# Optimization experiments

Hardware: AMD Instinct MI355X
Metric: run time of the kernel (lower is better)

The kernel has to match this reference:

```python
import jax, jax.numpy as jnp
import numpy as np

B, S, D = 2, 2048, 2048
HQ, HKV, HD = 32, 8, 64
G = HQ // HKV  # groups = 4


def _rope_freqs(seq_len, head_dim):
    # standard RoPE angles: theta_i = 10000^(-2i/d), angle[t,i] = t*theta_i
    inv = 1.0 / (10000.0 ** (np.arange(0, head_dim, 2, dtype=np.float32) / head_dim))
    ang = np.arange(seq_len, dtype=np.float32)[:, None] * inv[None, :]  # [S, HD/2]
    cos = np.cos(ang)[None, :, None, :]  # [1, S, 1, HD/2]
    sin = np.sin(ang)[None, :, None, :]
    return jnp.asarray(cos), jnp.asarray(sin)


def setup_inputs() -> dict:
    key = jax.random.key(0)
    ks = jax.random.split(key, 5)
    freq_cos, freq_sin = _rope_freqs(S, HD)
    scale_in = 1.0 / np.sqrt(D)
    return {
        "x": jax.random.normal(ks[0], (B, S, D), dtype=jnp.float32),
        "freq_cos": freq_cos,
        "freq_sin": freq_sin,
        "wq": jax.random.normal(ks[1], (D, HQ * HD), dtype=jnp.float32) * scale_in,
        "wk": jax.random.normal(ks[2], (D, HKV * HD), dtype=jnp.float32) * scale_in,
        "wv": jax.random.normal(ks[3], (D, HKV * HD), dtype=jnp.float32) * scale_in,
        "wo": jax.random.normal(ks[4], (HQ * HD, D), dtype=jnp.float32) * scale_in,
    }


def _apply_rope(x, cos, sin):
    # x: [b, s, h, hd]; treat last dim as hd/2 complex pairs (interleaved)
    b, s, h, d = x.shape
    xr = x[..., 0::2]  # real parts [b,s,h,hd/2]
    xi = x[..., 1::2]  # imag parts
    or_ = xr * cos - xi * sin
    oi_ = xr * sin + xi * cos
    return jnp.stack([or_, oi_], axis=-1).reshape(b, s, h, d)


def reference(x, freq_cos, freq_sin, wq, wk, wv, wo):
    b, s, d = x.shape
    q = (x @ wq).reshape(b, s, HQ, HD)
    k = (x @ wk).reshape(b, s, HKV, HD)
    v = (x @ wv).reshape(b, s, HKV, HD)
    q = _apply_rope(q, freq_cos[:, :s], freq_sin[:, :s])
    k = _apply_rope(k, freq_cos[:, :s], freq_sin[:, :s])
    # group query heads by kv head: [b, hkv, g, s, hd]
    q = q.transpose(0, 2, 1, 3).reshape(b, HKV, G, s, HD)
    k = k.transpose(0, 2, 1, 3)  # [b, hkv, s, hd]
    v = v.transpose(0, 2, 1, 3)  # [b, hkv, s, hd]
    scores = jnp.einsum("bkgqd,bktd->bkgqt", q, k)
    causal = jnp.tril(jnp.ones((s, s), dtype=bool))
    scores = jnp.where(causal, scores, -jnp.inf)
    attn = jax.nn.softmax(scores / np.sqrt(HD).astype(np.float32), axis=-1)
    out = jnp.einsum("bkgqt,bktd->bkgqd", attn, v)
    out = out.reshape(b, HQ, s, HD).transpose(0, 2, 1, 3).reshape(b, s, d)
    return out @ wo
```

## Files before the change

kernel.cpp:

```cpp
#include <hip/hip_runtime.h>

#define DEVI __device__ __forceinline__

typedef _Float16 h16;
typedef h16 h16x8 __attribute__((ext_vector_type(8)));
typedef h16 h16x4 __attribute__((ext_vector_type(4)));
typedef float f32x4 __attribute__((ext_vector_type(4)));
typedef unsigned short u16;
typedef u16 u16x8 __attribute__((ext_vector_type(8)));
typedef u16 u16x4 __attribute__((ext_vector_type(4)));

constexpr int Bc = 2, Sc = 2048, Dc = 2048, HQc = 32, HKVc = 8, HDc = 64;

DEVI u16 f2h(float f){ h16 h = (h16)f; return __builtin_bit_cast(u16, h); }
DEVI float h2f(u16 u){ return (float)__builtin_bit_cast(h16, u); }

DEVI f32x4 mfma32(h16x8 a, h16x8 b, f32x4 c){ return __builtin_amdgcn_mfma_f32_16x16x32_f16(a, b, c, 0, 0, 0); }
DEVI f32x4 mfma16(h16x4 a, h16x4 b, f32x4 c){ return __builtin_amdgcn_mfma_f32_16x16x16f16(a, b, c, 0, 0, 0); }

DEVI void glds16(const void* g, void* l){
  __builtin_amdgcn_global_load_lds((__attribute__((address_space(1))) void*)g,
                                   (__attribute__((address_space(3))) void*)l, 16, 0, 0);
}

__global__ __launch_bounds__(256) void convert_x(const float* __restrict__ src, u16* __restrict__ dst){
  size_t i = ((size_t)blockIdx.x * 256 + threadIdx.x) * 8;
  f32x4 a = *(const f32x4*)(src + i);
  f32x4 b = *(const f32x4*)(src + i + 4);
  u16x8 o;
  #pragma unroll
  for (int j = 0; j < 4; ++j){ o[j] = f2h(a[j]); o[4+j] = f2h(b[j]); }
  *(u16x8*)(dst + i) = o;
}

__global__ __launch_bounds__(256) void transpose_w(const float* __restrict__ wq, const float* __restrict__ wk,
                                                   const float* __restrict__ wv, const float* __restrict__ wo,
                                                   u16* __restrict__ wqT, u16* __restrict__ wkT,
                                                   u16* __restrict__ wvT, u16* __restrict__ woT){
  __shared__ float tile[32][33];
  int z = blockIdx.z;
  const float* src = (z==0) ? wq : (z==1) ? wk : (z==2) ? wv : wo;
  u16* dst         = (z==0) ? wqT : (z==1) ? wkT : (z==2) ? wvT : woT;
  int N = (z==0 || z==3) ? 2048 : 512;
  int n0 = blockIdx.x * 32;
  if (n0 >= N) return;
  int k0 = blockIdx.y * 32;
  int tx = threadIdx.x, ty = threadIdx.y;
  #pragma unroll
  for (int i = 0; i < 4; ++i)
    tile[ty + i*8][tx] = src[(size_t)(k0 + ty + i*8) * N + n0 + tx];
  __syncthreads();
  #pragma unroll
  for (int i = 0; i < 4; ++i){
    int nn = ty + i*8;
    dst[(size_t)(n0 + nn) * 2048 + k0 + tx] = f2h(tile[tx][nn]);
  }
}

template<int MODE>
__global__ __launch_bounds__(256) void gemm_k(const u16* __restrict__ A,
    const u16* __restrict__ W0, const u16* __restrict__ W1, const u16* __restrict__ W2,
    u16* __restrict__ Qb, u16* __restrict__ Kb, u16* __restrict__ Vb, float* __restrict__ Out){
  __shared__ u16 ldsA[128 * 64];
  __shared__ u16 ldsB[128 * 64];
  int tid = threadIdx.x, wv_ = tid >> 6, l = tid & 63, t = l & 15, g = l >> 4;
  int wm = wv_ >> 1, wn = wv_ & 1;
  int m0 = blockIdx.y * 128, n0 = blockIdx.x * 128;
  const u16* Wt; int n0l; int matid;
  if (MODE == 1){ Wt = W0; n0l = n0; matid = 0; }
  else {
    if (n0 < 2048)      { Wt = W0; n0l = n0;        matid = 0; }
    else if (n0 < 2560) { Wt = W1; n0l = n0 - 2048; matid = 1; }
    else                { Wt = W2; n0l = n0 - 2560; matid = 2; }
  }
  f32x4 acc[4][4] = {};
  int lr = l >> 3, lc = l & 7;
  for (int kk = 0; kk < 32; ++kk){
    int k0 = kk * 64;
    #pragma unroll
    for (int i = 0; i < 4; ++i){
      int row = wv_ * 32 + i * 8 + lr;
      int ca = lc ^ (row & 7);
      glds16(A  + (size_t)(m0  + row) * 2048 + k0 + ca * 8, &ldsA[(wv_*32 + i*8) * 64]);
      glds16(Wt + (size_t)(n0l + row) * 2048 + k0 + ca * 8, &ldsB[(wv_*32 + i*8) * 64]);
    }
    __syncthreads();
    #pragma unroll
    for (int kf = 0; kf < 2; ++kf){
      h16x8 af[4], bf[4];
      #pragma unroll
      for (int mb = 0; mb < 4; ++mb){
        int r = wm*64 + mb*16 + t;
        af[mb] = *(const h16x8*)&ldsA[r*64 + ((((kf<<2)|g) ^ (r&7)) << 3)];
      }
      #pragma unroll
      for (int nb = 0; nb < 4; ++nb){
        int r = wn*64 + nb*16 + t;
        bf[nb] = *(const h16x8*)&ldsB[r*64 + ((((kf<<2)|g) ^ (r&7)) << 3)];
      }
      #pragma unroll
      for (int mb = 0; mb < 4; ++mb)
        #pragma unroll
        for (int nb = 0; nb < 4; ++nb)
          acc[mb][nb] = mfma32(af[mb], bf[nb], acc[mb][nb]);
    }
    __syncthreads();
  }
  if (MODE == 0){
    #pragma unroll
    for (int mb = 0; mb < 4; ++mb){
      int mrow = m0 + wm*64 + mb*16 + (g << 2);
      #pragma unroll
      for (int nb = 0; nb < 4; ++nb){
        int col = n0l + wn*64 + nb*16 + t;
        int h = col >> 6, d = col & 63;
        #pragma unroll
        for (int r = 0; r < 4; ++r){
          int m = mrow + r;
          int bb = m >> 11, s = m & 2047;
          u16 v = f2h(acc[mb][nb][r]);
          if (matid == 0)      Qb[(((size_t)bb*HQc  + h)*Sc + s)*HDc + d] = v;
          else if (matid == 1) Kb[(((size_t)bb*HKVc + h)*Sc + s)*HDc + d] = v;
          else                 Vb[(((size_t)bb*HKVc + h)*Sc + s)*HDc + d] = v;
        }
      }
    }
  } else {
    #pragma unroll
    for (int mb = 0; mb < 4; ++mb){
      int mrow = m0 + wm*64 + mb*16 + (g << 2);
      #pragma unroll
      for (int nb = 0; nb < 4; ++nb){
        int col = n0 + wn*64 + nb*16 + t;
        #pragma unroll
        for (int r = 0; r < 4; ++r)
          Out[(size_t)(mrow + r) * 2048 + col] = acc[mb][nb][r];
      }
    }
  }
}

__global__ __launch_bounds__(256) void rope_k(u16* __restrict__ Qb, u16* __restrict__ Kb,
                                              const float* __restrict__ fcos, const float* __restrict__ fsin){
  int gid = blockIdx.x * 256 + threadIdx.x;
  int row = gid >> 3, seg = gid & 7;
  u16* p; float scale; int s;
  if (row < Bc*HQc*Sc){ p = Qb + (size_t)row*HDc + seg*8; s = row & (Sc-1); scale = 0.125f; }
  else { int r2 = row - Bc*HQc*Sc; p = Kb + (size_t)r2*HDc + seg*8; s = r2 & (Sc-1); scale = 1.0f; }
  u16x8 u = *(u16x8*)p;
  const float* cp = fcos + s*32 + seg*4;
  const float* sp = fsin + s*32 + seg*4;
  u16x8 o;
  #pragma unroll
  for (int i = 0; i < 4; ++i){
    float xr = h2f(u[2*i]), xi = h2f(u[2*i+1]);
    float c = cp[i], sn = sp[i];
    o[2*i]   = f2h((xr*c - xi*sn) * scale);
    o[2*i+1] = f2h((xr*sn + xi*c) * scale);
  }
  *(u16x8*)p = o;
}

__global__ __launch_bounds__(256) void attn_k(const u16* __restrict__ Qb, const u16* __restrict__ Kb,
                                              const u16* __restrict__ Vb, u16* __restrict__ Ob){
  __shared__ u16 vlds[64 * 36];
  int tid = threadIdx.x, w = tid >> 6, l = tid & 63, t = l & 15, g = l >> 4;
  int qb = blockIdx.x, head = blockIdx.y;
  int b = head >> 5, hq = head & 31, hkv = hq >> 2;
  int q0 = qb * 64;
  int qrow = q0 + w*16 + t;
  const u16* Qp = Qb + (((size_t)(b*HQc + hq))*Sc + qrow) * HDc;
  h16x8 qf0 = *(const h16x8*)(Qp + g*8);
  h16x8 qf1 = *(const h16x8*)(Qp + 32 + g*8);
  const u16* Kp = Kb + ((size_t)(b*HKVc + hkv)) * Sc * HDc;
  const u16* Vp = Vb + ((size_t)(b*HKVc + hkv)) * Sc * HDc;
  f32x4 o[4] = {};
  float m_run = -1e30f, l_run = 0.0f;
  const float LOG2E = 1.44269504f;
  int ntiles = qb*2 + 2;
  for (int tile = 0; tile < ntiles; ++tile){
    int kv0 = tile * 32;
    h16x8 ka00 = *(const h16x8*)(Kp + (size_t)(kv0      + t)*HDc +      g*8);
    h16x8 ka01 = *(const h16x8*)(Kp + (size_t)(kv0      + t)*HDc + 32 + g*8);
    h16x8 ka10 = *(const h16x8*)(Kp + (size_t)(kv0 + 16 + t)*HDc +      g*8);
    h16x8 ka11 = *(const h16x8*)(Kp + (size_t)(kv0 + 16 + t)*HDc + 32 + g*8);
    __syncthreads();
    {
      int kvi = tid >> 3, dseg = tid & 7;
      u16x8 v8 = *(const u16x8*)(Vp + (size_t)(kv0 + kvi)*HDc + dseg*8);
      #pragma unroll
      for (int j = 0; j < 8; ++j) vlds[(dseg*8 + j)*36 + kvi] = v8[j];
    }
    __syncthreads();
    f32x4 s0 = {}, s1 = {};
    s0 = mfma32(ka00, qf0, s0); s0 = mfma32(ka01, qf1, s0);
    s1 = mfma32(ka10, qf0, s1); s1 = mfma32(ka11, qf1, s1);
    float p0[4], p1[4];
    float mt = -1e30f;
    #pragma unroll
    for (int r = 0; r < 4; ++r){
      int kv = kv0 + (g<<2) + r;
      float x = (kv <= qrow) ? s0[r] : -1e30f;
      p0[r] = x; mt = fmaxf(mt, x);
    }
    #pragma unroll
    for (int r = 0; r < 4; ++r){
      int kv = kv0 + 16 + (g<<2) + r;
      float x = (kv <= qrow) ? s1[r] : -1e30f;
      p1[r] = x; mt = fmaxf(mt, x);
    }
    mt = fmaxf(mt, __shfl_xor(mt, 16));
    mt = fmaxf(mt, __shfl_xor(mt, 32));
    float m_new = fmaxf(m_run, mt);
    float alpha = exp2f((m_run - m_new) * LOG2E);
    float rs = 0.0f;
    #pragma unroll
    for (int r = 0; r < 4; ++r){ p0[r] = exp2f((p0[r] - m_new)*LOG2E); rs += p0[r]; }
    #pragma unroll
    for (int r = 0; r < 4; ++r){ p1[r] = exp2f((p1[r] - m_new)*LOG2E); rs += p1[r]; }
    rs += __shfl_xor(rs, 16); rs += __shfl_xor(rs, 32);
    l_run = l_run * alpha + rs;
    m_run = m_new;
    #pragma unroll
    for (int db = 0; db < 4; ++db)
      #pragma unroll
      for (int r = 0; r < 4; ++r) o[db][r] *= alpha;
    h16x4 pf0, pf1;
    #pragma unroll
    for (int j = 0; j < 4; ++j){ pf0[j] = (h16)p0[j]; pf1[j] = (h16)p1[j]; }
    #pragma unroll
    for (int db = 0; db < 4; ++db){
      const u16* vp = &vlds[(db*16 + t)*36 + (g<<2)];
      h16x4 vf0 = *(const h16x4*)vp;
      h16x4 vf1 = *(const h16x4*)(vp + 16);
      o[db] = mfma16(vf0, pf0, o[db]);
      o[db] = mfma16(vf1, pf1, o[db]);
    }
  }
  float inv = 1.0f / l_run;
  u16* Op = Ob + ((size_t)(b*Sc + qrow)) * Dc + hq*HDc;
  #pragma unroll
  for (int db = 0; db < 4; ++db){
    u16x4 st;
    #pragma unroll
    for (int r = 0; r < 4; ++r) st[r] = f2h(o[db][r] * inv);
    *(u16x4*)(Op + db*16 + (g<<2)) = st;
  }
}

extern "C" void kernel_launch(void* const* d_in, const int* in_sizes, int n_in,
                              void* d_out, int out_size, void* d_ws, size_t ws_size,
                              hipStream_t stream){
  const float* x    = (const float*)d_in[0];
  const float* fcos = (const float*)d_in[1];
  const float* fsin = (const float*)d_in[2];
  const float* wq   = (const float*)d_in[3];
  const float* wk   = (const float*)d_in[4];
  const float* wv   = (const float*)d_in[5];
  const float* wo   = (const float*)d_in[6];
  float* out = (float*)d_out;

  u16* ws  = (u16*)d_ws;
  u16* x16 = ws;
  u16* wqT = x16 + 8388608;
  u16* wkT = wqT + 4194304;
  u16* wvT = wkT + 1048576;
  u16* woT = wvT + 1048576;
  u16* Qb  = woT + 4194304;
  u16* Kb  = Qb  + 8388608;
  u16* Vb  = Kb  + 2097152;
  u16* Ob  = x16;

  convert_x  <<<4096, 256, 0, stream>>>(x, x16);
  transpose_w<<<dim3(64,64,4), dim3(32,8), 0, stream>>>(wq, wk, wv, wo, wqT, wkT, wvT, woT);
  gemm_k<0>  <<<dim3(24,32), 256, 0, stream>>>(x16, wqT, wkT, wvT, Qb, Kb, Vb, nullptr);
  rope_k     <<<5120, 256, 0, stream>>>(Qb, Kb, fcos, fsin);
  attn_k     <<<dim3(32,64), 256, 0, stream>>>(Qb, Kb, Vb, Ob);
  gemm_k<1>  <<<dim3(16,32), 256, 0, stream>>>(Ob, woT, nullptr, nullptr, nullptr, nullptr, nullptr, out);
}
```

Baseline: 505.3 us.

## Pair causal query tiles per block and double-buffer V in attention

Each attention block now handles two query tiles, fold and 31-fold, so work per block is even under the causal mask and the grid shrinks to half. V tiles are prefetched into a double-buffered LDS transpose with packed 32-bit stores, cutting one barrier per tile. The log2e factor is folded into the Q scaling at RoPE time. The kernel skips the causal mask on fully visible tiles, rescales lazily only when the running max grows by more than 8, and converts probabilities with packed RTZ. Lazy rescaling and RTZ rounding slightly change numerics, and fewer blocks may lower occupancy.

After: 519.2 us. 1.03x slower.

```diff
diff --git a/kernel.cpp b/kernel.cpp
--- a/kernel.cpp
+++ b/kernel.cpp
@@ -5,6 +5,7 @@
 typedef _Float16 h16;
 typedef h16 h16x8 __attribute__((ext_vector_type(8)));
 typedef h16 h16x4 __attribute__((ext_vector_type(4)));
+typedef h16 h16x2 __attribute__((ext_vector_type(2)));
 typedef float f32x4 __attribute__((ext_vector_type(4)));
 typedef unsigned short u16;
 typedef u16 u16x8 __attribute__((ext_vector_type(8)));
@@ -14,6 +15,7 @@
 
 DEVI u16 f2h(float f){ h16 h = (h16)f; return __builtin_bit_cast(u16, h); }
 DEVI float h2f(u16 u){ return (float)__builtin_bit_cast(h16, u); }
+DEVI h16x2 pkrtz(float a, float b){ return __builtin_bit_cast(h16x2, __builtin_amdgcn_cvt_pkrtz(a, b)); }
 
 DEVI f32x4 mfma32(h16x8 a, h16x8 b, f32x4 c){ return __builtin_amdgcn_mfma_f32_16x16x32_f16(a, b, c, 0, 0, 0); }
 DEVI f32x4 mfma16(h16x4 a, h16x4 b, f32x4 c){ return __builtin_amdgcn_mfma_f32_16x16x16f16(a, b, c, 0, 0, 0); }
@@ -145,7 +147,7 @@
   int gid = blockIdx.x * 256 + threadIdx.x;
   int row = gid >> 3, seg = gid & 7;
   u16* p; float scale; int s;
-  if (row < Bc*HQc*Sc){ p = Qb + (size_t)row*HDc + seg*8; s = row & (Sc-1); scale = 0.125f; }
+  if (row < Bc*HQc*Sc){ p = Qb + (size_t)row*HDc + seg*8; s = row & (Sc-1); scale = 0.125f * 1.44269504f; }
   else { int r2 = row - Bc*HQc*Sc; p = Kb + (size_t)r2*HDc + seg*8; s = r2 & (Sc-1); scale = 1.0f; }
   u16x8 u = *(u16x8*)p;
   const float* cp = fcos + s*32 + seg*4;
@@ -163,88 +165,120 @@
 
 __global__ __launch_bounds__(256) void attn_k(const u16* __restrict__ Qb, const u16* __restrict__ Kb,
                                               const u16* __restrict__ Vb, u16* __restrict__ Ob){
-  __shared__ u16 vlds[64 * 36];
+  __shared__ u16 vlds[2][64 * 34];
   int tid = threadIdx.x, w = tid >> 6, l = tid & 63, t = l & 15, g = l >> 4;
-  int qb = blockIdx.x, head = blockIdx.y;
+  int fold = blockIdx.x, head = blockIdx.y;
   int b = head >> 5, hq = head & 31, hkv = hq >> 2;
-  int q0 = qb * 64;
-  int qrow = q0 + w*16 + t;
-  const u16* Qp = Qb + (((size_t)(b*HQc + hq))*Sc + qrow) * HDc;
-  h16x8 qf0 = *(const h16x8*)(Qp + g*8);
-  h16x8 qf1 = *(const h16x8*)(Qp + 32 + g*8);
   const u16* Kp = Kb + ((size_t)(b*HKVc + hkv)) * Sc * HDc;
   const u16* Vp = Vb + ((size_t)(b*HKVc + hkv)) * Sc * HDc;
-  f32x4 o[4] = {};
-  float m_run = -1e30f, l_run = 0.0f;
-  const float LOG2E = 1.44269504f;
-  int ntiles = qb*2 + 2;
-  for (int tile = 0; tile < ntiles; ++tile){
-    int kv0 = tile * 32;
-    h16x8 ka00 = *(const h16x8*)(Kp + (size_t)(kv0      + t)*HDc +      g*8);
-    h16x8 ka01 = *(const h16x8*)(Kp + (size_t)(kv0      + t)*HDc + 32 + g*8);
-    h16x8 ka10 = *(const h16x8*)(Kp + (size_t)(kv0 + 16 + t)*HDc +      g*8);
-    h16x8 ka11 = *(const h16x8*)(Kp + (size_t)(kv0 + 16 + t)*HDc + 32 + g*8);
+  int kv2 = tid >> 4, dseg = tid & 15;
+
+  #pragma unroll 1
+  for (int part = 0; part < 2; ++part){
+    int qb = part ? (31 - fold) : fold;
+    int q0 = qb * 64, nt = 2*qb + 2;
+    int qrow = q0 + w*16 + t;
+    const u16* Qp = Qb + (((size_t)(b*HQc + hq))*Sc + qrow) * HDc;
+    h16x8 qf0 = *(const h16x8*)(Qp + g*8);
+    h16x8 qf1 = *(const h16x8*)(Qp + 32 + g*8);
+    f32x4 o[4] = {};
+    float m_run = -1e30f, l_run = 0.0f;
+
+    {
+      u16x4 a = *(const u16x4*)(Vp + (size_t)(2*kv2    )*HDc + dseg*4);
+      u16x4 c = *(const u16x4*)(Vp + (size_t)(2*kv2 + 1)*HDc + dseg*4);
+      #pragma unroll
+      for (int e = 0; e < 4; ++e){
+        unsigned pk = (unsigned)a[e] | ((unsigned)c[e] << 16);
+        *(unsigned*)&vlds[0][(dseg*4 + e)*34 + 2*kv2] = pk;
+      }
+    }
     __syncthreads();
-    {
-      int kvi = tid >> 3, dseg = tid & 7;
-      u16x8 v8 = *(const u16x8*)(Vp + (size_t)(kv0 + kvi)*HDc + dseg*8);
-      #pragma unroll
-      for (int j = 0; j < 8; ++j) vlds[(dseg*8 + j)*36 + kvi] = v8[j];
-    }
-    __syncthreads();
-    f32x4 s0 = {}, s1 = {};
-    s0 = mfma32(ka00, qf0, s0); s0 = mfma32(ka01, qf1, s0);
-    s1 = mfma32(ka10, qf0, s1); s1 = mfma32(ka11, qf1, s1);
-    float p0[4], p1[4];
-    float mt = -1e30f;
-    #pragma unroll
-    for (int r = 0; r < 4; ++r){
-      int kv = kv0 + (g<<2) + r;
-      float x = (kv <= qrow) ? s0[r] : -1e30f;
-      p0[r] = x; mt = fmaxf(mt, x);
-    }
-    #pragma unroll
-    for (int r = 0; r < 4; ++r){
-      int kv = kv0 + 16 + (g<<2) + r;
-      float x = (kv <= qrow) ? s1[r] : -1e30f;
-      p1[r] = x; mt = fmaxf(mt, x);
-    }
-    mt = fmaxf(mt, __shfl_xor(mt, 16));
-    mt = fmaxf(mt, __shfl_xor(mt, 32));
-    float m_new = fmaxf(m_run, mt);
-    float alpha = exp2f((m_run - m_new) * LOG2E);
-    float rs = 0.0f;
-    #pragma unroll
-    for (int r = 0; r < 4; ++r){ p0[r] = exp2f((p0[r] - m_new)*LOG2E); rs += p0[r]; }
-    #pragma unroll
-    for (int r = 0; r < 4; ++r){ p1[r] = exp2f((p1[r] - m_new)*LOG2E); rs += p1[r]; }
-    rs += __shfl_xor(rs, 16); rs += __shfl_xor(rs, 32);
-    l_run = l_run * alpha + rs;
-    m_run = m_new;
-    #pragma unroll
-    for (int db = 0; db < 4; ++db)
-      #pragma unroll
-      for (int r = 0; r < 4; ++r) o[db][r] *= alpha;
-    h16x4 pf0, pf1;
-    #pragma unroll
-    for (int j = 0; j < 4; ++j){ pf0[j] = (h16)p0[j]; pf1[j] = (h16)p1[j]; }
+
+    #pragma unroll 1
+    for (int tt = 0; tt < nt; ++tt){
+      int kv0 = tt * 32, cur = tt & 1;
+      bool have = (tt + 1 < nt);
+      u16x4 nv0, nv1;
+      if (have){
+        nv0 = *(const u16x4*)(Vp + (size_t)(kv0 + 32 + 2*kv2)*HDc + dseg*4);
+        nv1 = *(const u16x4*)(Vp + (size_t)(kv0 + 33 + 2*kv2)*HDc + dseg*4);
+      }
+      h16x8 ka00 = *(const h16x8*)(Kp + (size_t)(kv0      + t)*HDc +      g*8);
+      h16x8 ka01 = *(const h16x8*)(Kp + (size_t)(kv0      + t)*HDc + 32 + g*8);
+      h16x8 ka10 = *(const h16x8*)(Kp + (size_t)(kv0 + 16 + t)*HDc +      g*8);
+      h16x8 ka11 = *(const h16x8*)(Kp + (size_t)(kv0 + 16 + t)*HDc + 32 + g*8);
+      f32x4 s0 = {}, s1 = {};
+      s0 = mfma32(ka00, qf0, s0); s0 = mfma32(ka01, qf1, s0);
+      s1 = mfma32(ka10, qf0, s1); s1 = mfma32(ka11, qf1, s1);
+
+      float p0[4], p1[4];
+      if (tt >= 2*qb){
+        #pragma unroll
+        for (int r = 0; r < 4; ++r){
+          p0[r] = (kv0      + (g<<2) + r <= qrow) ? s0[r] : -1e30f;
+          p1[r] = (kv0 + 16 + (g<<2) + r <= qrow) ? s1[r] : -1e30f;
+        }
+      } else {
+        #pragma unroll
+        for (int r = 0; r < 4; ++r){ p0[r] = s0[r]; p1[r] = s1[r]; }
+      }
+      float mt = fmaxf(fmaxf(fmaxf(p0[0],p0[1]), fmaxf(p0[2],p0[3])),
+                       fmaxf(fmaxf(p1[0],p1[1]), fmaxf(p1[2],p1[3])));
+      mt = fmaxf(mt, __shfl_xor(mt, 16));
+      mt = fmaxf(mt, __shfl_xor(mt, 32));
+      if (!__all(mt <= m_run + 8.0f)){
+        float m_new = fmaxf(m_run, mt);
+        float alpha = exp2f(m_run - m_new);
+        l_run *= alpha;
+        #pragma unroll
+        for (int db = 0; db < 4; ++db)
+          #pragma unroll
+          for (int r = 0; r < 4; ++r) o[db][r] *= alpha;
+        m_run = m_new;
+      }
+      float rs = 0.0f;
+      #pragma unroll
+      for (int r = 0; r < 4; ++r){ p0[r] = exp2f(p0[r] - m_run); rs += p0[r]; }
+      #pragma unroll
+      for (int r = 0; r < 4; ++r){ p1[r] = exp2f(p1[r] - m_run); rs += p1[r]; }
+      rs += __shfl_xor(rs, 16); rs += __shfl_xor(rs, 32);
+      l_run += rs;
+
+      if (have){
+        #pragma unroll
+        for (int e = 0; e < 4; ++e){
+          unsigned pk = (unsigned)nv0[e] | ((unsigned)nv1[e] << 16);
+          *(unsigned*)&vlds[cur^1][(dseg*4 + e)*34 + 2*kv2] = pk;
+        }
+      }
+
+      h16x2 c0 = pkrtz(p0[0], p0[1]);
+      h16x2 c1 = pkrtz(p0[2], p0[3]);
+      h16x2 c2 = pkrtz(p1[0], p1[1]);
+      h16x2 c3 = pkrtz(p1[2], p1[3]);
+      h16x4 pf0 = {c0[0], c0[1], c1[0], c1[1]};
+      h16x4 pf1 = {c2[0], c2[1], c3[0], c3[1]};
+      #pragma unroll
+      for (int db = 0; db < 4; ++db){
+        const u16* vp = &vlds[cur][(db*16 + t)*34 + (g<<2)];
+        h16x4 vf0 = *(const h16x4*)vp;
+        h16x4 vf1 = *(const h16x4*)(vp + 16);
+        o[db] = mfma16(vf0, pf0, o[db]);
+        o[db] = mfma16(vf1, pf1, o[db]);
+      }
+      __syncthreads();
+    }
+
+    float inv = 1.0f / l_run;
+    u16* Op = Ob + ((size_t)(b*Sc + qrow)) * Dc + hq*HDc;
     #pragma unroll
     for (int db = 0; db < 4; ++db){
-      const u16* vp = &vlds[(db*16 + t)*36 + (g<<2)];
-      h16x4 vf0 = *(const h16x4*)vp;
-      h16x4 vf1 = *(const h16x4*)(vp + 16);
-      o[db] = mfma16(vf0, pf0, o[db]);
-      o[db] = mfma16(vf1, pf1, o[db]);
-    }
-  }
-  float inv = 1.0f / l_run;
-  u16* Op = Ob + ((size_t)(b*Sc + qrow)) * Dc + hq*HDc;
-  #pragma unroll
-  for (int db = 0; db < 4; ++db){
-    u16x4 st;
-    #pragma unroll
-    for (int r = 0; r < 4; ++r) st[r] = f2h(o[db][r] * inv);
-    *(u16x4*)(Op + db*16 + (g<<2)) = st;
+      u16x4 st;
+      #pragma unroll
+      for (int r = 0; r < 4; ++r) st[r] = f2h(o[db][r] * inv);
+      *(u16x4*)(Op + db*16 + (g<<2)) = st;
+    }
   }
 }
 
@@ -275,6 +309,6 @@
   transpose_w<<<dim3(64,64,4), dim3(32,8), 0, stream>>>(wq, wk, wv, wo, wqT, wkT, wvT, woT);
   gemm_k<0>  <<<dim3(24,32), 256, 0, stream>>>(x16, wqT, wkT, wvT, Qb, Kb, Vb, nullptr);
   rope_k     <<<5120, 256, 0, stream>>>(Qb, Kb, fcos, fsin);
-  attn_k     <<<dim3(32,64), 256, 0, stream>>>(Qb, Kb, Vb, Ob);
+  attn_k     <<<dim3(16,64), 256, 0, stream>>>(Qb, Kb, Vb, Ob);
   gemm_k<1>  <<<dim3(16,32), 256, 0, stream>>>(Ob, woT, nullptr, nullptr, nullptr, nullptr, nullptr, out);
 }
```
